# Performance work log

Hardware: AMD Instinct MI355X
Metric: run time of the kernel (lower is better)

Reference implementation:

```python
import jax, jax.numpy as jnp
import numpy as np

N_NODES = 40000
EMB = 256
NHEADS = 2
HEAD = EMB // NHEADS
NLAYERS = 4
NGNN = 2
LN_EPS = 1e-5
LEAKY = 0.01


def setup_inputs() -> dict:
    key = jax.random.key(0)
    ks = iter(jax.random.split(key, 40))
    nrm = lambda shape, s=0.05: jax.random.normal(next(ks), shape, dtype=jnp.float32) * s
    inp = {
        'feat0': nrm((20000, 512), 1.0),
        'feat1': nrm((20000, 512), 1.0),
        'fc_w0': nrm((256, 512)), 'fc_b0': jnp.zeros((256,), jnp.float32),
        'fc_w1': nrm((256, 512)), 'fc_b1': jnp.zeros((256,), jnp.float32),
        'gcn_w': nrm((NGNN, 256, 256)),
        'edge_src': jax.random.randint(next(ks), (640000,), 0, N_NODES),
        'edge_dst': jax.random.randint(next(ks), (640000,), 0, N_NODES),
        'dg_seqs': jax.random.randint(next(ks), (1024, 64), 0, N_NODES),
        'pt_seqs': jax.random.randint(next(ks), (1024, 64), 0, N_NODES),
        'type_emb': nrm((4, 4), 1.0),
        'node_type': jax.random.randint(next(ks), (N_NODES,), 0, 4),
        'gt_wl': nrm((8, 256, 256)), 'gt_wr': nrm((8, 256, 256)),
        'gt_al': nrm((8, 1, HEAD)), 'gt_ar': nrm((8, 1, HEAD)),
        'gt_wf': nrm((8, 256, 256)),
        'ln_g': jnp.ones((8, 256), jnp.float32), 'ln_b': jnp.zeros((8, 256), jnp.float32),
        'proj_d_w': nrm((2, 256, 256)), 'proj_d_b': jnp.zeros((2, 256), jnp.float32),
        'proj_p_w': nrm((2, 256, 256)), 'proj_p_b': jnp.zeros((2, 256), jnp.float32),
        'ml_w1': nrm((256, 512)), 'ml_b1': jnp.zeros((256,), jnp.float32),
        'ml_w2': nrm((128, 256)), 'ml_b2': jnp.zeros((128,), jnp.float32),
        'ml_w3': nrm((1, 128)), 'ml_b3': jnp.zeros((1,), jnp.float32),
    }
    return inp


def _layernorm(x, g, b):
    m = x.mean(-1, keepdims=True)
    v = ((x - m) ** 2).mean(-1, keepdims=True)
    return (x - m) * jax.lax.rsqrt(v + LN_EPS) * g + b


def _leaky(x):
    return jnp.where(x >= 0, x, LEAKY * x)


def _agt_layer(h, wl, wr, al, ar, wf, g, b):
    # h: [B, L, EMB]; additive (GAT-style) attention, temper = 1.0
    B, L, _ = h.shape
    fl = (h @ wl.T).reshape(B, L, NHEADS, HEAD).transpose(0, 2, 1, 3)  # [B,H,L,hd]
    fr = (h @ wr.T).reshape(B, L, NHEADS, HEAD).transpose(0, 2, 1, 3)
    sl = _leaky(fl) @ al.T                     # [B,H,L,1]
    sr = _leaky(fr) @ ar.T                     # [B,H,L,1]
    score = jax.nn.softmax(sl + sr.transpose(0, 1, 3, 2), axis=-1)  # [B,H,L,L]
    ctx = score @ fr                           # [B,H,L,hd]
    h_sa = ctx.transpose(0, 2, 1, 3).reshape(B, L, EMB)
    return _layernorm(h + h_sa @ wf.T, g, b)


def _gcn(gh, W, src, dst):
    # DGL GraphConv norm='both', allow_zero_in_degree, activation=relu
    ones = jnp.ones(src.shape[0], gh.dtype)
    deg_out = jnp.clip(jax.ops.segment_sum(ones, src, num_segments=N_NODES), 1.0)
    deg_in = jnp.clip(jax.ops.segment_sum(ones, dst, num_segments=N_NODES), 1.0)
    x = gh * (deg_out ** -0.5)[:, None]
    x = x @ W
    agg = jax.ops.segment_sum(x[src], dst, num_segments=N_NODES)
    return jax.nn.relu(agg * (deg_in ** -0.5)[:, None])


def reference(feat0, feat1, fc_w0, fc_b0, fc_w1, fc_b1, gcn_w, edge_src, edge_dst,
              dg_seqs, pt_seqs, type_emb, node_type, gt_wl, gt_wr, gt_al, gt_ar,
              gt_wf, ln_g, ln_b, proj_d_w, proj_d_b, proj_p_w, proj_p_b,
              ml_w1, ml_b1, ml_w2, ml_b2, ml_w3, ml_b3):
    # per-type input projections, concatenated along node dim
    h0 = feat0 @ fc_w0.T + fc_b0
    h1 = feat1 @ fc_w1.T + fc_b1
    gh = jnp.concatenate([h0, h1], axis=0)  # [N, EMB]
    r = type_emb[node_type]                 # computed but unused downstream (faithful)
    for layer in range(NGNN):
        gh = _gcn(gh, gcn_w[layer], edge_src, edge_dst)
    # graph transformer per node type (dropout = identity in eval)
    embs = []
    for t, seqs in ((0, dg_seqs), (1, pt_seqs)):
        h = gh[seqs]                        # [B, L, EMB]
        _ = r[seqs]
        for l in range(NLAYERS):
            i = t * NLAYERS + l
            h = _agt_layer(h, gt_wl[i], gt_wr[i], gt_al[i], gt_ar[i], gt_wf[i], ln_g[i], ln_b[i])
        embs.append(h[:, 0, :])
    dg_emb, pt_emb = embs
    # Proj heads: linear -> elu -> linear
    dg_emb = jax.nn.elu(dg_emb @ proj_d_w[0].T + proj_d_b[0]) @ proj_d_w[1].T + proj_d_b[1]
    pt_emb = jax.nn.elu(pt_emb @ proj_p_w[0].T + proj_p_b[0]) @ proj_p_w[1].T + proj_p_b[1]
    # Predict MLP on concat
    x = jnp.concatenate([dg_emb, pt_emb], axis=1)  # [B, 512]
    x = jax.nn.relu(x @ ml_w1.T + ml_b1)
    x = jax.nn.relu(x @ ml_w2.T + ml_b2)
    out = jax.nn.sigmoid(x @ ml_w3.T + ml_b3)
    return out.reshape(x.shape[0])
```

## Files before the change

### kernel.cpp

```cpp
#include <hip/hip_runtime.h>
#include <hip/hip_bf16.h>
#include <math.h>

typedef unsigned int u32;
typedef unsigned short u16;
typedef __attribute__((ext_vector_type(8))) short bf16x8;
typedef __attribute__((ext_vector_type(4))) float f32x4;

__device__ __forceinline__ float b2f(u16 u) { union { u32 i; float f; } c; c.i = ((u32)u) << 16; return c.f; }
__device__ __forceinline__ u16 f2b(float f) { __hip_bfloat16 h = __float2bfloat16(f); u16 r; __builtin_memcpy(&r, &h, 2); return r; }
__device__ __forceinline__ float b2f_lo(u32 w) { union { u32 i; float f; } c; c.i = w << 16; return c.f; }
__device__ __forceinline__ float b2f_hi(u32 w) { union { u32 i; float f; } c; c.i = w & 0xffff0000u; return c.f; }
__device__ __forceinline__ u32 pk2(float a, float b) { return (u32)f2b(a) | ((u32)f2b(b) << 16); }

__device__ __forceinline__ float wave_sum(float v) {
    #pragma unroll
    for (int off = 32; off > 0; off >>= 1) v += __shfl_xor(v, off, 64);
    return v;
}

template<int CTRL>
__device__ __forceinline__ float dpp_addf(float v) {
    int y = __builtin_amdgcn_update_dpp(0, __builtin_bit_cast(int, v), CTRL, 0xF, 0xF, true);
    return v + __builtin_bit_cast(float, y);
}
template<int CTRL>
__device__ __forceinline__ float dpp_movf(float v) {
    int y = __builtin_amdgcn_update_dpp(0, __builtin_bit_cast(int, v), CTRL, 0xF, 0xF, true);
    return __builtin_bit_cast(float, y);
}
__device__ __forceinline__ float sum16_dpp(float v) {
    v = dpp_addf<0xB1>(v);
    v = dpp_addf<0x4E>(v);
    v = dpp_addf<0x141>(v);
    v = dpp_addf<0x140>(v);
    return v;
}
__device__ __forceinline__ float sum8_dpp(float v) {
    v = dpp_addf<0xB1>(v);
    v = dpp_addf<0x4E>(v);
    v = dpp_addf<0x141>(v);
    return v;
}

template<bool AF32>
__global__ __launch_bounds__(256) void mfma_gemm_kernel(
    const void* __restrict__ Av, const u16* __restrict__ B,
    const float* __restrict__ bias, const float* __restrict__ rowscale,
    u16* __restrict__ Cb, int M, int N, int K,
    const void* __restrict__ Av1, const u16* __restrict__ B1,
    const float* __restrict__ bias1, u16* __restrict__ Cb1)
{
    if (blockIdx.z) { Av = Av1; B = B1; bias = bias1; Cb = Cb1; }
    __shared__ u16 lds[(64 + 128) * 64];
    const int tid = threadIdx.x;
    const int wid = tid >> 6, lane = tid & 63;
    const int wr = wid >> 1, wc = wid & 1;
    const int m0 = blockIdx.y * 64, n0 = blockIdx.x * 128;

    f32x4 acc[2][4] = {};

    for (int k0 = 0; k0 < K; k0 += 64) {
        #pragma unroll
        for (int s = 0; s < 2; ++s) {
            int idx = tid + s * 256;
            int row = idx >> 3, g = idx & 7;
            int row_g = m0 + row; if (row_g >= M) row_g = M - 1;
            int swz = ((g << 4) ^ ((row & 7) << 4));
            if (AF32) {
                const float* src = (const float*)Av + (size_t)row_g * K + k0 + g * 8;
                float4 v0 = *(const float4*)src;
                float4 v1 = *(const float4*)(src + 4);
                uint4 pk;
                pk.x = pk2(v0.x, v0.y); pk.y = pk2(v0.z, v0.w);
                pk.z = pk2(v1.x, v1.y); pk.w = pk2(v1.z, v1.w);
                *(uint4*)((char*)lds + row * 128 + swz) = pk;
            } else {
                f32x4 v = *(const f32x4*)((const u16*)Av + (size_t)row_g * K + k0 + g * 8);
                *(f32x4*)((char*)lds + row * 128 + swz) = v;
            }
        }
        #pragma unroll
        for (int s = 0; s < 4; ++s) {
            int idx = tid + s * 256;
            int row = idx >> 3, g = idx & 7;
            int row_g = n0 + row; if (row_g >= N) row_g = N - 1;
            f32x4 v = *(const f32x4*)(B + (size_t)row_g * K + k0 + g * 8);
            *(f32x4*)((char*)lds + 8192 + row * 128 + ((g << 4) ^ ((row & 7) << 4))) = v;
        }
        __syncthreads();
        #pragma unroll
        for (int ks = 0; ks < 2; ++ks) {
            const int off = (ks * 64 + ((lane >> 4) << 4)) ^ ((lane & 7) << 4);
            const int ra = lane & 15;
            bf16x8 af[2], bfr[4];
            #pragma unroll
            for (int i = 0; i < 2; ++i)
                af[i] = *(bf16x8*)((char*)lds + (wr * 32 + i * 16 + ra) * 128 + off);
            #pragma unroll
            for (int j = 0; j < 4; ++j)
                bfr[j] = *(bf16x8*)((char*)lds + 8192 + (wc * 64 + j * 16 + ra) * 128 + off);
            #pragma unroll
            for (int i = 0; i < 2; ++i)
                #pragma unroll
                for (int j = 0; j < 4; ++j)
                    acc[i][j] = __builtin_amdgcn_mfma_f32_16x16x32_bf16(af[i], bfr[j], acc[i][j], 0, 0, 0);
        }
        __syncthreads();
    }

    const int cr = lane >> 4, ccol = lane & 15;
    #pragma unroll
    for (int i = 0; i < 2; ++i) {
        #pragma unroll
        for (int j = 0; j < 4; ++j) {
            int colg = n0 + wc * 64 + j * 16 + ccol;
            if (colg >= N) continue;
            float badd = bias ? bias[colg] : 0.f;
            #pragma unroll
            for (int reg = 0; reg < 4; ++reg) {
                int rowg = m0 + wr * 32 + i * 16 + cr * 4 + reg;
                if (rowg >= M) continue;
                float v = acc[i][j][reg] + badd;
                if (rowscale) v *= rowscale[rowg];
                Cb[(size_t)rowg * N + colg] = f2b(v);
            }
        }
    }
}

__global__ __launch_bounds__(512, 4) void fused_transformer_kernel(
    const float* __restrict__ gh, const int* __restrict__ dg_seqs,
    const int* __restrict__ pt_seqs,
    const u16* __restrict__ wrN,
    const u16* __restrict__ wfN,
    const float* __restrict__ ar,
    const float* __restrict__ lng, const float* __restrict__ lnb,
    float* __restrict__ embT)
{
    __shared__ u16 ldsA[64 * 256];
    __shared__ float scoreH[2][64];
    __shared__ __align__(16) u32 ctxB[128];
    __shared__ __align__(16) float uS[256];

    const int tid = threadIdx.x;
    const int bx = blockIdx.x;
    const int t = bx >> 10, s = bx & 1023;
    const int r = tid >> 3, o8 = tid & 7;
    const int wid = tid >> 6, lane = tid & 63;
    const int hd = wid >> 2;
    const int g4 = lane >> 4, cl = lane & 15;

    const int* seqs = t ? pt_seqs : dg_seqs;

    float4 y[8];
    {
        int node = seqs[s * 64 + r];
        const float* src = gh + (size_t)node * 256 + o8 * 32;
        #pragma unroll
        for (int v = 0; v < 8; ++v) y[v] = *(const float4*)(src + v * 4);
    }

    for (int l = 0; l < 4; ++l) {
        const int li = t * 4 + l;

        {
            const int c = o8 >> 1, gb = (o8 & 1) * 4;
            #pragma unroll
            for (int gg = 0; gg < 4; ++gg) {
                float4 a = y[2 * gg], b = y[2 * gg + 1];
                uint4 pk;
                pk.x = pk2(a.x, a.y); pk.y = pk2(a.z, a.w);
                pk.z = pk2(b.x, b.y); pk.w = pk2(b.z, b.w);
                int g = gb + gg;
                int off = ((g << 4) ^ ((r & 7) << 4)) ^ (c << 4);
                *(uint4*)((char*)ldsA + c * 8192 + r * 128 + off) = pk;
            }
            if (tid < 128) ((float*)scoreH)[tid] = 0.f;
        }
        __syncthreads();

        f32x4 acc[4][2] = {};
        {
            const u16* wrl = wrN + (size_t)li * 65536;
            const int ra = lane & 15;
            #pragma unroll
            for (int kc = 0; kc < 8; ++kc) {
                const int c = kc >> 1, ks = kc & 1;
                const int off = ((ks * 64 + ((lane >> 4) << 4)) ^ ((lane & 7) << 4)) ^ (c << 4);
                bf16x8 af[4], bfr[2];
                #pragma unroll
                for (int i = 0; i < 4; ++i)
                    af[i] = *(bf16x8*)((char*)ldsA + c * 8192 + (i * 16 + ra) * 128 + off);
                #pragma unroll
                for (int j = 0; j < 2; ++j)
                    bfr[j] = *(const bf16x8*)(wrl + ((size_t)((wid * 2 + j) * 8 + kc) << 9) + lane * 8);
                #pragma unroll
                for (int i = 0; i < 4; ++i)
                    #pragma unroll
                    for (int j = 0; j < 2; ++j)
                        acc[i][j] = __builtin_amdgcn_mfma_f32_16x16x32_bf16(af[i], bfr[j], acc[i][j], 0, 0, 0);
            }
        }

        {
            const float* arl = ar + li * 128;
            float arj[2];
            #pragma unroll
            for (int j = 0; j < 2; ++j) arj[j] = arl[(wid & 3) * 32 + j * 16 + cl];
            #pragma unroll
            for (int i = 0; i < 4; ++i)
                #pragma unroll
                for (int reg = 0; reg < 4; ++reg) {
                    float sc;
                    {
                        float x0 = acc[i][0][reg], x1 = acc[i][1][reg];
                        sc = (x0 >= 0.f ? x0 : 0.01f * x0) * arj[0]
                           + (x1 >= 0.f ? x1 : 0.01f * x1) * arj[1];
                    }
                    sc = sum16_dpp(sc);
                    if (cl == 0) atomicAdd(&scoreH[hd][i * 16 + g4 * 4 + reg], sc);
                }
        }
        __syncthreads();

        float p[4][4];
        {
            const float* sc = scoreH[hd];
            #pragma unroll
            for (int i = 0; i < 4; ++i)
                *(float4*)p[i] = *(const float4*)(sc + i * 16 + g4 * 4);
            float mx = -1e30f;
            #pragma unroll
            for (int i = 0; i < 4; ++i)
                #pragma unroll
                for (int reg = 0; reg < 4; ++reg) mx = fmaxf(mx, p[i][reg]);
            mx = fmaxf(mx, __shfl_xor(mx, 16, 64));
            mx = fmaxf(mx, __shfl_xor(mx, 32, 64));
            float sme = 0.f;
            #pragma unroll
            for (int i = 0; i < 4; ++i)
                #pragma unroll
                for (int reg = 0; reg < 4; ++reg) {
                    p[i][reg] = __expf(p[i][reg] - mx);
                    sme += p[i][reg];
                }
            sme += __shfl_xor(sme, 16, 64);
            sme += __shfl_xor(sme, 32, 64);
            float inv = 1.f / sme;
            #pragma unroll
            for (int i = 0; i < 4; ++i)
                #pragma unroll
                for (int reg = 0; reg < 4; ++reg) p[i][reg] *= inv;
        }

        {
            #pragma unroll
            for (int j = 0; j < 2; ++j) {
                float c = 0.f;
                #pragma unroll
                for (int i = 0; i < 4; ++i)
                    #pragma unroll
                    for (int reg = 0; reg < 4; ++reg)
                        c = fmaf(p[i][reg], acc[i][j][reg], c);
                c += __shfl_xor(c, 16, 64);
                c += __shfl_xor(c, 32, 64);
                float cn = dpp_movf<0xB1>(c);
                if (g4 == 0 && (cl & 1) == 0)
                    ctxB[wid * 16 + j * 8 + (cl >> 1)] = pk2(c, cn);
            }
        }
        __syncthreads();

        {
            const u16* wfl = wfN + (size_t)li * 65536;
            f32x4 au0 = {}, au1 = {};
            #pragma unroll
            for (int kc = 0; kc < 8; ++kc) {
                bf16x8 cf = *(bf16x8*)((char*)ctxB + kc * 64 + ((lane >> 4) << 4));
                bf16x8 w0 = *(const bf16x8*)(wfl + ((size_t)((wid * 2 + 0) * 8 + kc) << 9) + lane * 8);
                bf16x8 w1 = *(const bf16x8*)(wfl + ((size_t)((wid * 2 + 1) * 8 + kc) << 9) + lane * 8);
                au0 = __builtin_amdgcn_mfma_f32_16x16x32_bf16(cf, w0, au0, 0, 0, 0);
                au1 = __builtin_amdgcn_mfma_f32_16x16x32_bf16(cf, w1, au1, 0, 0, 0);
            }
            if (lane < 16) {
                uS[wid * 32 + lane] = au0[0];
                uS[wid * 32 + 16 + lane] = au1[0];
            }
        }
        __syncthreads();

        {
            #pragma unroll
            for (int v = 0; v < 8; ++v) {
                float4 uv = *(const float4*)&uS[o8 * 32 + v * 4];
                y[v].x += uv.x; y[v].y += uv.y; y[v].z += uv.z; y[v].w += uv.w;
            }
            float sm = 0.f, qq = 0.f;
            #pragma unroll
            for (int v = 0; v < 8; ++v) {
                sm += y[v].x + y[v].y + y[v].z + y[v].w;
                qq += y[v].x * y[v].x + y[v].y * y[v].y + y[v].z * y[v].z + y[v].w * y[v].w;
            }
            sm = sum8_dpp(sm);
            qq = sum8_dpp(qq);
            float mean = sm * (1.f / 256.f);
            float var = qq * (1.f / 256.f) - mean * mean;
            float inv = rsqrtf(var + 1e-5f);
            const float* gl = lng + li * 256 + o8 * 32;
            const float* bl = lnb + li * 256 + o8 * 32;
            if (l < 3) {
                #pragma unroll
                for (int v = 0; v < 8; ++v) {
                    float4 gv = *(const float4*)(gl + v * 4);
                    float4 bv = *(const float4*)(bl + v * 4);
                    y[v].x = (y[v].x - mean) * inv * gv.x + bv.x;
                    y[v].y = (y[v].y - mean) * inv * gv.y + bv.y;
                    y[v].z = (y[v].z - mean) * inv * gv.z + bv.z;
                    y[v].w = (y[v].w - mean) * inv * gv.w + bv.w;
                }
            } else if (r == 0) {
                float* dst = embT + (size_t)(t * 1024 + s) * 256 + o8 * 32;
                #pragma unroll
                for (int v = 0; v < 8; ++v) {
                    float4 gv = *(const float4*)(gl + v * 4);
                    float4 bv = *(const float4*)(bl + v * 4);
                    float4 o;
                    o.x = (y[v].x - mean) * inv * gv.x + bv.x;
                    o.y = (y[v].y - mean) * inv * gv.y + bv.y;
                    o.z = (y[v].z - mean) * inv * gv.z + bv.z;
                    o.w = (y[v].w - mean) * inv * gv.w + bv.w;
                    *(float4*)(dst + v * 4) = o;
                }
            }
        }
    }
}

template<bool BT>
__global__ __launch_bounds__(256) void gemm_kernel(
    const float* __restrict__ A, const float* __restrict__ B,
    const float* __restrict__ bias, const float* __restrict__ rowscale,
    float* __restrict__ C,
    int M, int N, int K, int lda, int ldb, int ldc, int coff, int act,
    const float* __restrict__ A1, const float* __restrict__ B1,
    const float* __restrict__ bias1, float* __restrict__ C1, int coff1)
{
    if (blockIdx.z) { A = A1; B = B1; bias = bias1; C = C1; coff = coff1; }
    __shared__ float As[32][64 + 4];
    __shared__ float Bs[32][64 + 4];
    const int tid = threadIdx.x;
    const int m0 = blockIdx.y * 64;
    const int n0 = blockIdx.x * 64;
    const int ty = tid >> 4, tx = tid & 15;
    float acc[4][4] = {};
    for (int k0 = 0; k0 < K; k0 += 32) {
        #pragma unroll
        for (int r = 0; r < 2; ++r) {
            int f4 = tid + r * 256;
            int arw = f4 >> 3, af = (f4 & 7) << 2;
            float4 v = make_float4(0.f, 0.f, 0.f, 0.f);
            int grow = m0 + arw;
            if (grow < M) {
                v = *(const float4*)(A + (size_t)grow * lda + k0 + af);
                if (rowscale) { float s = rowscale[grow]; v.x *= s; v.y *= s; v.z *= s; v.w *= s; }
            }
            As[af + 0][arw] = v.x; As[af + 1][arw] = v.y; As[af + 2][arw] = v.z; As[af + 3][arw] = v.w;
        }
        #pragma unroll
        for (int r = 0; r < 2; ++r) {
            int f4 = tid + r * 256;
            int col = f4 >> 3, kf = (f4 & 7) << 2;
            float4 v = make_float4(0.f, 0.f, 0.f, 0.f);
            if (n0 + col < N) v = *(const float4*)(B + (size_t)(n0 + col) * ldb + k0 + kf);
            Bs[kf + 0][col] = v.x; Bs[kf + 1][col] = v.y; Bs[kf + 2][col] = v.z; Bs[kf + 3][col] = v.w;
        }
        __syncthreads();
        #pragma unroll
        for (int kk = 0; kk < 32; ++kk) {
            float4 a4 = *(const float4*)&As[kk][ty << 2];
            float4 b4 = *(const float4*)&Bs[kk][tx << 2];
            float a[4] = {a4.x, a4.y, a4.z, a4.w};
            float b[4] = {b4.x, b4.y, b4.z, b4.w};
            #pragma unroll
            for (int i = 0; i < 4; ++i)
                #pragma unroll
                for (int j = 0; j < 4; ++j)
                    acc[i][j] = fmaf(a[i], b[j], acc[i][j]);
        }
        __syncthreads();
    }
    #pragma unroll
    for (int i = 0; i < 4; ++i) {
        int row = m0 + (ty << 2) + i;
        if (row >= M) continue;
        #pragma unroll
        for (int j = 0; j < 4; ++j) {
            int col = n0 + (tx << 2) + j;
            if (col >= N) continue;
            float v = acc[i][j];
            if (bias) v += bias[col];
            if (act == 1) v = fmaxf(v, 0.f);
            else if (act == 2) v = (v > 0.f) ? v : expm1f(v);
            C[(size_t)row * ldc + coff + col] = v;
        }
    }
}

#define EDGE_CAP 128
__global__ __launch_bounds__(256) void conv_all_kernel(
    const float* __restrict__ fc_w0, const float* __restrict__ fc_w1,
    const float* __restrict__ gcn_w, const float* __restrict__ gt_wr,
    const float* __restrict__ gt_wf,
    u16* __restrict__ fcw_b, u16* __restrict__ gcnw_b,
    u16* __restrict__ wrN, u16* __restrict__ wfN,
    const int* __restrict__ esrc, const int* __restrict__ edst,
    int* __restrict__ ebuf, int* __restrict__ cursor, int* __restrict__ cnt_out)
{
    int bid = blockIdx.x, tid = threadIdx.x;
    if (bid < 256) {
        const float* src = bid < 128 ? fc_w0 : fc_w1;
        u16* dst = fcw_b + (bid < 128 ? 0 : 131072);
        int i = ((bid & 127) * 256 + tid) * 4;
        float4 v = *(const float4*)(src + i);
        *(uint2*)(dst + i) = make_uint2(pk2(v.x, v.y), pk2(v.z, v.w));
    } else if (bid < 768) {
        int idx = (bid - 256) * 256 + tid;
        int l = idx >> 16, rem = idx & 65535;
        int k = rem >> 8, n = rem & 255;
        gcnw_b[(size_t)l * 65536 + n * 256 + k] = f2b(gcn_w[(size_t)l * 65536 + k * 256 + n]);
    } else if (bid < 1280) {
        const float* w = bid < 1024 ? gt_wr : gt_wf;
        u16* dst = bid < 1024 ? wrN : wfN;
        int idx = ((bid & 255)) * 256 + tid;
        int lane = idx & 63;
        int kc = (idx >> 6) & 7;
        int gn = (idx >> 9) & 15;
        int l = idx >> 13;
        int row = gn * 16 + (lane & 15);
        int k0 = kc * 32 + (lane >> 4) * 8;
        const float* src = w + ((size_t)l * 256 + row) * 256 + k0;
        float4 v0 = *(const float4*)src;
        float4 v1 = *(const float4*)(src + 4);
        uint4 pk;
        pk.x = pk2(v0.x, v0.y); pk.y = pk2(v0.z, v0.w);
        pk.z = pk2(v1.x, v1.y); pk.w = pk2(v1.z, v1.w);
        *(uint4*)(dst + (size_t)idx * 8) = pk;
    } else {
        int e0 = ((bid - 1280) * 256 + tid) * 4;
        if (e0 >= 640000) return;
        int4 s4 = *(const int4*)(esrc + e0);
        int4 d4 = *(const int4*)(edst + e0);
        atomicAdd(&cnt_out[s4.x], 1);
        atomicAdd(&cnt_out[s4.y], 1);
        atomicAdd(&cnt_out[s4.z], 1);
        atomicAdd(&cnt_out[s4.w], 1);
        int p0 = atomicAdd(&cursor[d4.x], 1);
        int p1 = atomicAdd(&cursor[d4.y], 1);
        int p2 = atomicAdd(&cursor[d4.z], 1);
        int p3 = atomicAdd(&cursor[d4.w], 1);
        if (p0 < EDGE_CAP) ebuf[(size_t)d4.x * EDGE_CAP + p0] = s4.x;
        if (p1 < EDGE_CAP) ebuf[(size_t)d4.y * EDGE_CAP + p1] = s4.y;
        if (p2 < EDGE_CAP) ebuf[(size_t)d4.z * EDGE_CAP + p2] = s4.z;
        if (p3 < EDGE_CAP) ebuf[(size_t)d4.w * EDGE_CAP + p3] = s4.w;
    }
}

__global__ __launch_bounds__(256) void deg_fin_kernel(const int* __restrict__ cnt, float* __restrict__ dinv, int n) {
    int i = blockIdx.x * 256 + threadIdx.x;
    if (i < n) dinv[i] = rsqrtf(fmaxf((float)cnt[i], 1.0f));
}

template<bool WF, bool WB>
__global__ __launch_bounds__(256) void csr_agg_kernel(
    const u16* __restrict__ x, const int* __restrict__ ebuf,
    const int* __restrict__ deg, float* __restrict__ outf, u16* __restrict__ outb, int nnodes)
{
    int n = blockIdx.x * 4 + (threadIdx.x >> 6);
    if (n >= nnodes) return;
    int lane = threadIdx.x & 63;
    int d = deg[n];
    float dinv = rsqrtf(fmaxf((float)d, 1.0f));
    if (d > EDGE_CAP) d = EDGE_CAP;
    const int* eb = ebuf + (size_t)n * EDGE_CAP;
    const int co = lane << 2;
    float a0 = 0.f, a1 = 0.f, a2 = 0.f, a3 = 0.f;
    int k = 0;
    for (; k + 4 <= d; k += 4) {
        int4 s4 = *(const int4*)(eb + k);
        uint2 va = *(const uint2*)(x + (size_t)s4.x * 256 + co);
        uint2 vb = *(const uint2*)(x + (size_t)s4.y * 256 + co);
        uint2 vc = *(const uint2*)(x + (size_t)s4.z * 256 + co);
        uint2 vd = *(const uint2*)(x + (size_t)s4.w * 256 + co);
        a0 += b2f_lo(va.x) + b2f_lo(vb.x) + b2f_lo(vc.x) + b2f_lo(vd.x);
        a1 += b2f_hi(va.x) + b2f_hi(vb.x) + b2f_hi(vc.x) + b2f_hi(vd.x);
        a2 += b2f_lo(va.y) + b2f_lo(vb.y) + b2f_lo(vc.y) + b2f_lo(vd.y);
        a3 += b2f_hi(va.y) + b2f_hi(vb.y) + b2f_hi(vc.y) + b2f_hi(vd.y);
    }
    for (; k < d; ++k) {
        int s = eb[k];
        uint2 v = *(const uint2*)(x + (size_t)s * 256 + co);
        a0 += b2f_lo(v.x); a1 += b2f_hi(v.x);
        a2 += b2f_lo(v.y); a3 += b2f_hi(v.y);
    }
    a0 = fmaxf(a0 * dinv, 0.f); a1 = fmaxf(a1 * dinv, 0.f);
    a2 = fmaxf(a2 * dinv, 0.f); a3 = fmaxf(a3 * dinv, 0.f);
    if (WF) *(float4*)(outf + (size_t)n * 256 + co) = make_float4(a0, a1, a2, a3);
    if (WB) *(uint2*)(outb + (size_t)n * 256 + co) = make_uint2(pk2(a0, a1), pk2(a2, a3));
}

__global__ __launch_bounds__(256) void mlp_tail_kernel(
    const float* __restrict__ m1, const float* __restrict__ w2,
    const float* __restrict__ b2, const float* __restrict__ w3,
    const float* __restrict__ b3, float* __restrict__ out)
{
    __shared__ float rowS[4][256];
    const int w = threadIdx.x >> 6, lane = threadIdx.x & 63;
    const int row = blockIdx.x * 4 + w;
    *(float4*)&rowS[w][lane * 4] = *(const float4*)(m1 + (size_t)row * 256 + lane * 4);
    __syncthreads();
    const float* rp = rowS[w];
    float v0 = b2[lane], v1 = b2[64 + lane];
    const float* wa = w2 + (size_t)lane * 256;
    const float* wb = w2 + (size_t)(64 + lane) * 256;
    #pragma unroll 8
    for (int d = 0; d < 256; d += 4) {
        float4 rv = *(const float4*)(rp + d);
        float4 a = *(const float4*)(wa + d);
        float4 b = *(const float4*)(wb + d);
        v0 = fmaf(rv.x, a.x, v0); v0 = fmaf(rv.y, a.y, v0);
        v0 = fmaf(rv.z, a.z, v0); v0 = fmaf(rv.w, a.w, v0);
        v1 = fmaf(rv.x, b.x, v1); v1 = fmaf(rv.y, b.y, v1);
        v1 = fmaf(rv.z, b.z, v1); v1 = fmaf(rv.w, b.w, v1);
    }
    v0 = fmaxf(v0, 0.f); v1 = fmaxf(v1, 0.f);
    float s = v0 * w3[lane] + v1 * w3[64 + lane];
    s = wave_sum(s);
    if (lane == 0) out[row] = 1.f / (1.f + expf(-(s + b3[0])));
}

static inline int cdiv(int a, int b) { return (a + b - 1) / b; }

extern "C" void kernel_launch(void* const* d_in, const int* in_sizes, int n_in,
                              void* d_out, int out_size, void* d_ws, size_t ws_size,
                              hipStream_t stream)
{
    const float* feat0   = (const float*)d_in[0];
    const float* feat1   = (const float*)d_in[1];
    const float* fc_w0   = (const float*)d_in[2];
    const float* fc_b0   = (const float*)d_in[3];
    const float* fc_w1   = (const float*)d_in[4];
    const float* fc_b1   = (const float*)d_in[5];
    const float* gcn_w   = (const float*)d_in[6];
    const int*   edge_src= (const int*)d_in[7];
    const int*   edge_dst= (const int*)d_in[8];
    const int*   dg_seqs = (const int*)d_in[9];
    const int*   pt_seqs = (const int*)d_in[10];
    const float* gt_wr   = (const float*)d_in[14];
    const float* gt_ar   = (const float*)d_in[16];
    const float* gt_wf   = (const float*)d_in[17];
    const float* ln_g    = (const float*)d_in[18];
    const float* ln_b    = (const float*)d_in[19];
    const float* proj_d_w= (const float*)d_in[20];
    const float* proj_d_b= (const float*)d_in[21];
    const float* proj_p_w= (const float*)d_in[22];
    const float* proj_p_b= (const float*)d_in[23];
    const float* ml_w1   = (const float*)d_in[24];
    const float* ml_b1   = (const float*)d_in[25];
    const float* ml_w2   = (const float*)d_in[26];
    const float* ml_b2   = (const float*)d_in[27];
    const float* ml_w3   = (const float*)d_in[28];
    const float* ml_b3   = (const float*)d_in[29];
    float* out = (float*)d_out;

    float* base  = (float*)d_ws;
    float* gh    = base;
    float* gcnR  = gh + 10240000;
    float* dego  = gcnR + 15440000;
    float* embT  = dego + 40000;
    float* t1    = embT + 524288;
    float* mx    = t1 + 524288;
    float* m1    = mx + 524288;
    float* m2    = m1 + 262144;
    float* wreg  = m2 + 131072;

    u16* tmp_b   = (u16*)gcnR;
    int* ebuf    = (int*)(gcnR + 5120000);
    int* cursor  = ebuf + (size_t)40000 * EDGE_CAP;
    int* cnt_out = cursor + 40000;
    u16* gh_b    = (u16*)(gcnR + 10320000);

    u16* fcw_b   = (u16*)wreg;
    u16* gcnw_b  = fcw_b + 262144;
    u16* wrN     = gcnw_b + 131072;
    u16* wfN     = wrN + 524288;

    hipMemsetAsync(cursor, 0, 80000 * sizeof(int), stream);
    conv_all_kernel<<<1905, 256, 0, stream>>>(
        fc_w0, fc_w1, gcn_w, gt_wr, gt_wf, fcw_b, gcnw_b, wrN, wfN,
        edge_src, edge_dst, ebuf, cursor, cnt_out);
    deg_fin_kernel<<<cdiv(40000, 256), 256, 0, stream>>>(cnt_out, dego, 40000);

    mfma_gemm_kernel<true><<<dim3(2, cdiv(20000, 64), 2), 256, 0, stream>>>(
        feat0, fcw_b, fc_b0, nullptr, gh_b, 20000, 256, 512,
        feat1, fcw_b + 131072, fc_b1, gh_b + (size_t)20000 * 256);

    mfma_gemm_kernel<false><<<dim3(2, cdiv(40000, 64), 1), 256, 0, stream>>>(
        gh_b, gcnw_b, nullptr, dego, tmp_b, 40000, 256, 256,
        gh_b, gcnw_b, nullptr, tmp_b);
    csr_agg_kernel<false, true><<<10000, 256, 0, stream>>>(tmp_b, ebuf, cursor, gh, gh_b, 40000);
    mfma_gemm_kernel<false><<<dim3(2, cdiv(40000, 64), 1), 256, 0, stream>>>(
        gh_b, gcnw_b + 65536, nullptr, dego, tmp_b, 40000, 256, 256,
        gh_b, gcnw_b, nullptr, tmp_b);
    csr_agg_kernel<true, false><<<10000, 256, 0, stream>>>(tmp_b, ebuf, cursor, gh, gh_b, 40000);

    fused_transformer_kernel<<<2048, 512, 0, stream>>>(
        gh, dg_seqs, pt_seqs, wrN, wfN, gt_ar, ln_g, ln_b, embT);

    gemm_kernel<true><<<dim3(4, 16, 2), 256, 0, stream>>>(
        embT, proj_d_w, proj_d_b, nullptr, t1, 1024, 256, 256, 256, 256, 256, 0, 2,
        embT + 262144, proj_p_w, proj_p_b, t1 + 262144, 0);
    gemm_kernel<true><<<dim3(4, 16, 2), 256, 0, stream>>>(
        t1, proj_d_w + 65536, proj_d_b + 256, nullptr, mx, 1024, 256, 256, 256, 256, 512, 0, 0,
        t1 + 262144, proj_p_w + 65536, proj_p_b + 256, mx, 256);

    gemm_kernel<true><<<dim3(4, 16, 1), 256, 0, stream>>>(
        mx, ml_w1, ml_b1, nullptr, m1, 1024, 256, 512, 512, 512, 256, 0, 1,
        mx, ml_w1, ml_b1, m1, 0);
    mlp_tail_kernel<<<256, 256, 0, stream>>>(m1, ml_w2, ml_b2, ml_w3, ml_b3, out);
}
```

Before: 601.2 us.

## Fuse projection heads and prediction MLP into one per-row kernel; unroll CSR gather

Replaces the three tiled fp32 GEMM launches and the MLP tail kernel with a single kernel that runs one 256-thread block per batch row. Each block chains both projection heads, the first MLP layer, the second layer and the sigmoid entirely in LDS, with each thread doing a dot product against weight rows read from global memory. This removes three kernel launches and the intermediate global buffers, but every block re-reads all weight matrices, so reuse now depends on L2 rather than on tiling. The CSR aggregation loop is also unrolled from 4 to 8 neighbours per iteration to expose more outstanding gather loads.

```diff
diff --git a/kernel.cpp b/kernel.cpp
--- a/kernel.cpp
+++ b/kernel.cpp
@@ -41,6 +41,27 @@
     v = dpp_addf<0x4E>(v);
     v = dpp_addf<0x141>(v);
     return v;
+}
+
+template<int LEN>
+__device__ __forceinline__ float dot_lds(const float* __restrict__ v, const float* __restrict__ w, float acc) {
+    float a0 = acc, a1 = 0.f, a2 = 0.f, a3 = 0.f;
+    #pragma unroll
+    for (int d = 0; d < LEN; d += 16) {
+        float4 v0 = *(const float4*)(v + d),      w0 = *(const float4*)(w + d);
+        float4 v1 = *(const float4*)(v + d + 4),  w1 = *(const float4*)(w + d + 4);
+        float4 v2 = *(const float4*)(v + d + 8),  w2 = *(const float4*)(w + d + 8);
+        float4 v3 = *(const float4*)(v + d + 12), w3 = *(const float4*)(w + d + 12);
+        a0 = fmaf(v0.x, w0.x, a0); a0 = fmaf(v0.y, w0.y, a0);
+        a0 = fmaf(v0.z, w0.z, a0); a0 = fmaf(v0.w, w0.w, a0);
+        a1 = fmaf(v1.x, w1.x, a1); a1 = fmaf(v1.y, w1.y, a1);
+        a1 = fmaf(v1.z, w1.z, a1); a1 = fmaf(v1.w, w1.w, a1);
+        a2 = fmaf(v2.x, w2.x, a2); a2 = fmaf(v2.y, w2.y, a2);
+        a2 = fmaf(v2.z, w2.z, a2); a2 = fmaf(v2.w, w2.w, a2);
+        a3 = fmaf(v3.x, w3.x, a3); a3 = fmaf(v3.y, w3.y, a3);
+        a3 = fmaf(v3.z, w3.z, a3); a3 = fmaf(v3.w, w3.w, a3);
+    }
+    return (a0 + a1) + (a2 + a3);
 }
 
 template<bool AF32>
@@ -333,76 +354,6 @@
                     *(float4*)(dst + v * 4) = o;
                 }
             }
-        }
-    }
-}
-
-template<bool BT>
-__global__ __launch_bounds__(256) void gemm_kernel(
-    const float* __restrict__ A, const float* __restrict__ B,
-    const float* __restrict__ bias, const float* __restrict__ rowscale,
-    float* __restrict__ C,
-    int M, int N, int K, int lda, int ldb, int ldc, int coff, int act,
-    const float* __restrict__ A1, const float* __restrict__ B1,
-    const float* __restrict__ bias1, float* __restrict__ C1, int coff1)
-{
-    if (blockIdx.z) { A = A1; B = B1; bias = bias1; C = C1; coff = coff1; }
-    __shared__ float As[32][64 + 4];
-    __shared__ float Bs[32][64 + 4];
-    const int tid = threadIdx.x;
-    const int m0 = blockIdx.y * 64;
-    const int n0 = blockIdx.x * 64;
-    const int ty = tid >> 4, tx = tid & 15;
-    float acc[4][4] = {};
-    for (int k0 = 0; k0 < K; k0 += 32) {
-        #pragma unroll
-        for (int r = 0; r < 2; ++r) {
-            int f4 = tid + r * 256;
-            int arw = f4 >> 3, af = (f4 & 7) << 2;
-            float4 v = make_float4(0.f, 0.f, 0.f, 0.f);
-            int grow = m0 + arw;
-            if (grow < M) {
-                v = *(const float4*)(A + (size_t)grow * lda + k0 + af);
-                if (rowscale) { float s = rowscale[grow]; v.x *= s; v.y *= s; v.z *= s; v.w *= s; }
-            }
-            As[af + 0][arw] = v.x; As[af + 1][arw] = v.y; As[af + 2][arw] = v.z; As[af + 3][arw] = v.w;
-        }
-        #pragma unroll
-        for (int r = 0; r < 2; ++r) {
-            int f4 = tid + r * 256;
-            int col = f4 >> 3, kf = (f4 & 7) << 2;
-            float4 v = make_float4(0.f, 0.f, 0.f, 0.f);
-            if (n0 + col < N) v = *(const float4*)(B + (size_t)(n0 + col) * ldb + k0 + kf);
-            Bs[kf + 0][col] = v.x; Bs[kf + 1][col] = v.y; Bs[kf + 2][col] = v.z; Bs[kf + 3][col] = v.w;
-        }
-        __syncthreads();
-        #pragma unroll
-        for (int kk = 0; kk < 32; ++kk) {
-            float4 a4 = *(const float4*)&As[kk][ty << 2];
-            float4 b4 = *(const float4*)&Bs[kk][tx << 2];
-            float a[4] = {a4.x, a4.y, a4.z, a4.w};
-            float b[4] = {b4.x, b4.y, b4.z, b4.w};
-            #pragma unroll
-            for (int i = 0; i < 4; ++i)
-                #pragma unroll
-                for (int j = 0; j < 4; ++j)
-                    acc[i][j] = fmaf(a[i], b[j], acc[i][j]);
-        }
-        __syncthreads();
-    }
-    #pragma unroll
-    for (int i = 0; i < 4; ++i) {
-        int row = m0 + (ty << 2) + i;
-        if (row >= M) continue;
-        #pragma unroll
-        for (int j = 0; j < 4; ++j) {
-            int col = n0 + (tx << 2) + j;
-            if (col >= N) continue;
-            float v = acc[i][j];
-            if (bias) v += bias[col];
-            if (act == 1) v = fmaxf(v, 0.f);
-            else if (act == 2) v = (v > 0.f) ? v : expm1f(v);
-            C[(size_t)row * ldc + coff + col] = v;
         }
     }
 }
@@ -486,16 +437,25 @@
     const int co = lane << 2;
     float a0 = 0.f, a1 = 0.f, a2 = 0.f, a3 = 0.f;
     int k = 0;
-    for (; k + 4 <= d; k += 4) {
-        int4 s4 = *(const int4*)(eb + k);
-        uint2 va = *(const uint2*)(x + (size_t)s4.x * 256 + co);
-        uint2 vb = *(const uint2*)(x + (size_t)s4.y * 256 + co);
-        uint2 vc = *(const uint2*)(x + (size_t)s4.z * 256 + co);
-        uint2 vd = *(const uint2*)(x + (size_t)s4.w * 256 + co);
-        a0 += b2f_lo(va.x) + b2f_lo(vb.x) + b2f_lo(vc.x) + b2f_lo(vd.x);
-        a1 += b2f_hi(va.x) + b2f_hi(vb.x) + b2f_hi(vc.x) + b2f_hi(vd.x);
-        a2 += b2f_lo(va.y) + b2f_lo(vb.y) + b2f_lo(vc.y) + b2f_lo(vd.y);
-        a3 += b2f_hi(va.y) + b2f_hi(vb.y) + b2f_hi(vc.y) + b2f_hi(vd.y);
+    for (; k + 8 <= d; k += 8) {
+        int4 sA = *(const int4*)(eb + k);
+        int4 sB = *(const int4*)(eb + k + 4);
+        uint2 v0 = *(const uint2*)(x + (size_t)sA.x * 256 + co);
+        uint2 v1 = *(const uint2*)(x + (size_t)sA.y * 256 + co);
+        uint2 v2 = *(const uint2*)(x + (size_t)sA.z * 256 + co);
+        uint2 v3 = *(const uint2*)(x + (size_t)sA.w * 256 + co);
+        uint2 v4 = *(const uint2*)(x + (size_t)sB.x * 256 + co);
+        uint2 v5 = *(const uint2*)(x + (size_t)sB.y * 256 + co);
+        uint2 v6 = *(const uint2*)(x + (size_t)sB.z * 256 + co);
+        uint2 v7 = *(const uint2*)(x + (size_t)sB.w * 256 + co);
+        a0 += b2f_lo(v0.x) + b2f_lo(v1.x) + b2f_lo(v2.x) + b2f_lo(v3.x)
+            + b2f_lo(v4.x) + b2f_lo(v5.x) + b2f_lo(v6.x) + b2f_lo(v7.x);
+        a1 += b2f_hi(v0.x) + b2f_hi(v1.x) + b2f_hi(v2.x) + b2f_hi(v3.x)
+            + b2f_hi(v4.x) + b2f_hi(v5.x) + b2f_hi(v6.x) + b2f_hi(v7.x);
+        a2 += b2f_lo(v0.y) + b2f_lo(v1.y) + b2f_lo(v2.y) + b2f_lo(v3.y)
+            + b2f_lo(v4.y) + b2f_lo(v5.y) + b2f_lo(v6.y) + b2f_lo(v7.y);
+        a3 += b2f_hi(v0.y) + b2f_hi(v1.y) + b2f_hi(v2.y) + b2f_hi(v3.y)
+            + b2f_hi(v4.y) + b2f_hi(v5.y) + b2f_hi(v6.y) + b2f_hi(v7.y);
     }
     for (; k < d; ++k) {
         int s = eb[k];
@@ -509,34 +469,51 @@
     if (WB) *(uint2*)(outb + (size_t)n * 256 + co) = make_uint2(pk2(a0, a1), pk2(a2, a3));
 }
 
-__global__ __launch_bounds__(256) void mlp_tail_kernel(
-    const float* __restrict__ m1, const float* __restrict__ w2,
-    const float* __restrict__ b2, const float* __restrict__ w3,
-    const float* __restrict__ b3, float* __restrict__ out)
+__global__ __launch_bounds__(256) void head_tail_kernel(
+    const float* __restrict__ embT,
+    const float* __restrict__ pdw, const float* __restrict__ pdb,
+    const float* __restrict__ ppw, const float* __restrict__ ppb,
+    const float* __restrict__ w1, const float* __restrict__ b1,
+    const float* __restrict__ w2, const float* __restrict__ b2,
+    const float* __restrict__ w3, const float* __restrict__ b3,
+    float* __restrict__ out)
 {
-    __shared__ float rowS[4][256];
-    const int w = threadIdx.x >> 6, lane = threadIdx.x & 63;
-    const int row = blockIdx.x * 4 + w;
-    *(float4*)&rowS[w][lane * 4] = *(const float4*)(m1 + (size_t)row * 256 + lane * 4);
-    __syncthreads();
-    const float* rp = rowS[w];
-    float v0 = b2[lane], v1 = b2[64 + lane];
-    const float* wa = w2 + (size_t)lane * 256;
-    const float* wb = w2 + (size_t)(64 + lane) * 256;
-    #pragma unroll 8
-    for (int d = 0; d < 256; d += 4) {
-        float4 rv = *(const float4*)(rp + d);
-        float4 a = *(const float4*)(wa + d);
-        float4 b = *(const float4*)(wb + d);
-        v0 = fmaf(rv.x, a.x, v0); v0 = fmaf(rv.y, a.y, v0);
-        v0 = fmaf(rv.z, a.z, v0); v0 = fmaf(rv.w, a.w, v0);
-        v1 = fmaf(rv.x, b.x, v1); v1 = fmaf(rv.y, b.y, v1);
-        v1 = fmaf(rv.z, b.z, v1); v1 = fmaf(rv.w, b.w, v1);
-    }
-    v0 = fmaxf(v0, 0.f); v1 = fmaxf(v1, 0.f);
-    float s = v0 * w3[lane] + v1 * w3[64 + lane];
-    s = wave_sum(s);
-    if (lane == 0) out[row] = 1.f / (1.f + expf(-(s + b3[0])));
+    __shared__ float A[256], B[256], X[512];
+    const int n = threadIdx.x;
+    const int row = blockIdx.x;
+
+    A[n] = embT[(size_t)row * 256 + n];
+    __syncthreads();
+    {
+        float acc = dot_lds<256>(A, pdw + (size_t)n * 256, pdb[n]);
+        B[n] = acc > 0.f ? acc : expm1f(acc);
+    }
+    __syncthreads();
+    {
+        float aNext = embT[(size_t)(1024 + row) * 256 + n];
+        X[n] = dot_lds<256>(B, pdw + 65536 + (size_t)n * 256, pdb[256 + n]);
+        A[n] = aNext;
+    }
+    __syncthreads();
+    {
+        float acc = dot_lds<256>(A, ppw + (size_t)n * 256, ppb[n]);
+        B[n] = acc > 0.f ? acc : expm1f(acc);
+    }
+    __syncthreads();
+    X[256 + n] = dot_lds<256>(B, ppw + 65536 + (size_t)n * 256, ppb[256 + n]);
+    __syncthreads();
+    A[n] = fmaxf(dot_lds<512>(X, w1 + (size_t)n * 512, b1[n]), 0.f);
+    __syncthreads();
+    if (n < 128) {
+        float m2 = fmaxf(dot_lds<256>(A, w2 + (size_t)n * 256, b2[n]), 0.f);
+        B[n] = m2 * w3[n];
+    }
+    __syncthreads();
+    if (n < 64) {
+        float s = B[n] + B[64 + n];
+        s = wave_sum(s);
+        if (n == 0) out[row] = 1.f / (1.f + expf(-(s + b3[0])));
+    }
 }
 
 static inline int cdiv(int a, int b) { return (a + b - 1) / b; }
@@ -578,11 +555,7 @@
     float* gcnR  = gh + 10240000;
     float* dego  = gcnR + 15440000;
     float* embT  = dego + 40000;
-    float* t1    = embT + 524288;
-    float* mx    = t1 + 524288;
-    float* m1    = mx + 524288;
-    float* m2    = m1 + 262144;
-    float* wreg  = m2 + 131072;
+    float* wreg  = embT + 524288;
 
     u16* tmp_b   = (u16*)gcnR;
     int* ebuf    = (int*)(gcnR + 5120000);
@@ -617,15 +590,7 @@
     fused_transformer_kernel<<<2048, 512, 0, stream>>>(
         gh, dg_seqs, pt_seqs, wrN, wfN, gt_ar, ln_g, ln_b, embT);
 
-    gemm_kernel<true><<<dim3(4, 16, 2), 256, 0, stream>>>(
-        embT, proj_d_w, proj_d_b, nullptr, t1, 1024, 256, 256, 256, 256, 256, 0, 2,
-        embT + 262144, proj_p_w, proj_p_b, t1 + 262144, 0);
-    gemm_kernel<true><<<dim3(4, 16, 2), 256, 0, stream>>>(
-        t1, proj_d_w + 65536, proj_d_b + 256, nullptr, mx, 1024, 256, 256, 256, 256, 512, 0, 0,
-        t1 + 262144, proj_p_w + 65536, proj_p_b + 256, mx, 256);
-
-    gemm_kernel<true><<<dim3(4, 16, 1), 256, 0, stream>>>(
-        mx, ml_w1, ml_b1, nullptr, m1, 1024, 256, 512, 512, 512, 256, 0, 1,
-        mx, ml_w1, ml_b1, m1, 0);
-    mlp_tail_kernel<<<256, 256, 0, stream>>>(m1, ml_w2, ml_b2, ml_w3, ml_b3, out);
-}
+    head_tail_kernel<<<1024, 256, 0, stream>>>(
+        embT, proj_d_w, proj_d_b, proj_p_w, proj_p_b,
+        ml_w1, ml_b1, ml_w2, ml_b2, ml_w3, ml_b3, out);
+}
```

After: 691.3 us. +15.0%, slower.
